# Kernel optimization log

Measured on AMD Instinct MI355X. Metric: run time of the kernel, lower is better.

## Reference

```python
import jax, jax.numpy as jnp
import numpy as np

SIGMA = 0.4


def setup_inputs() -> dict:
    key = jax.random.key(0)
    k1, k2, k3 = jax.random.split(key, 3)
    B, T_out, T_in = 64, 2048, 512
    att_ws = jax.random.uniform(k1, (B, T_out, T_in), dtype=jnp.float32)
    ilens = jax.random.randint(k2, (B,), 1, T_in + 1, dtype=jnp.int64)
    olens = jax.random.randint(k3, (B,), 1, T_out + 1, dtype=jnp.int64)
    return {"att_ws": att_ws, "ilens": ilens, "olens": olens}


def reference(att_ws, ilens, olens):
    B, T_out, T_in = att_ws.shape
    dt = att_ws.dtype
    # grid_x indexes output frames (rows), grid_y indexes input tokens (cols)
    gx = jnp.arange(T_out, dtype=dt)[None, :, None]   # [1, T_out, 1]
    gy = jnp.arange(T_in, dtype=dt)[None, None, :]    # [1, 1, T_in]
    il = ilens.astype(dt)[:, None, None]              # [B, 1, 1]
    ol = olens.astype(dt)[:, None, None]
    # guided diagonal mask: 1 - exp(-(y/ilen - x/olen)^2 / (2 sigma^2))
    guided = 1.0 - jnp.exp(-((gy / il - gx / ol) ** 2) / (2.0 * SIGMA ** 2))
    # non-padded region per sample (out_mask & in_mask)
    valid = (gx < ol) & (gy < il)                     # [B, T_out, T_in] bool
    l1_err = jnp.where(valid, guided * att_ws, jnp.zeros((), dt))
    denom = olens.astype(dt)
    l1_mae = l1_err.sum(axis=(1, 2)) / denom
    l2_mse = (l1_err ** 2).sum(axis=(1, 2)) / denom
    return (l1_mae, l2_mse)
```

## Files before the change

kernel.cpp:

```cpp
#include <hip/hip_runtime.h>
#include <hip/hip_bf16.h>


#define GA_B     64
#define GA_TOUT  2048
#define GA_TIN   512
#define ROWS_PER_WAVE   8
#define WAVES_PER_BLOCK 4
#define ROWS_PER_BLOCK  (ROWS_PER_WAVE * WAVES_PER_BLOCK)
#define BLOCK_THREADS   256
#define GRID_X          (GA_TOUT / ROWS_PER_BLOCK)
#define KS 2.1233046f

__global__ __launch_bounds__(BLOCK_THREADS)
void ga_partial_kernel(const float* __restrict__ att,
                       const int* __restrict__ ilens,
                       const int* __restrict__ olens,
                       float* __restrict__ part) {
    const int b    = blockIdx.y;
    const int lane = threadIdx.x & 63;
    const int wave = threadIdx.x >> 6;
    const int waveRow = blockIdx.x * ROWS_PER_BLOCK + wave * ROWS_PER_WAVE;

    const int ol = olens[b];
    const int il = ilens[b];
    const int nv = (il + 3) >> 2;

    float l1 = 0.0f, l2 = 0.0f;

    if (waveRow < ol) {
        const float inv_il_s = KS / (float)il;
        const float inv_ol_s = KS / (float)ol;
        const bool  hi       = (nv > 64);
        const float4* __restrict__ base =
            (const float4*)(att + (size_t)b * GA_TOUT * GA_TIN);

        float ys0[4], ys1[4], m0[4], m1[4];
        #pragma unroll
        for (int j = 0; j < 4; ++j) {
            const int y0 = (lane << 2) + j;
            const int y1 = y0 + 256;
            ys0[j] = (float)y0 * inv_il_s;
            ys1[j] = (float)y1 * inv_il_s;
            m0[j]  = (y0 < il) ? 1.0f : 0.0f;
            m1[j]  = (y1 < il) ? 1.0f : 0.0f;
        }

        float4 A0[ROWS_PER_WAVE], A1[ROWS_PER_WAVE];
        #pragma unroll
        for (int r = 0; r < ROWS_PER_WAVE; ++r) {
            A0[r] = make_float4(0.f, 0.f, 0.f, 0.f);
            A1[r] = make_float4(0.f, 0.f, 0.f, 0.f);
            const int x = waveRow + r;
            if (x < ol) {
                const float4* __restrict__ rowp = base + (size_t)x * (GA_TIN / 4);
                if (lane < nv)              A0[r] = rowp[lane];
                if (hi && (lane + 64 < nv)) A1[r] = rowp[lane + 64];
            }
        }

        #pragma unroll
        for (int r = 0; r < ROWS_PER_WAVE; ++r) {
            const int   x   = waveRow + r;
            const float gxs = (float)x * inv_ol_s;
            {
                const float4 a = A0[r];
                #pragma unroll
                for (int j = 0; j < 4; ++j) {
                    const float av = (j == 0) ? a.x : (j == 1) ? a.y
                                   : (j == 2) ? a.z : a.w;
                    const float w  = ys0[j] - gxs;
                    const float E  = exp2f(-w * w);
                    const float q  = av - av * E;
                    const float e  = q * m0[j];
                    l1 += e;
                    l2 += e * e;
                }
            }
            if (hi) {
                const float4 a = A1[r];
                #pragma unroll
                for (int j = 0; j < 4; ++j) {
                    const float av = (j == 0) ? a.x : (j == 1) ? a.y
                                   : (j == 2) ? a.z : a.w;
                    const float w  = ys1[j] - gxs;
                    const float E  = exp2f(-w * w);
                    const float q  = av - av * E;
                    const float e  = q * m1[j];
                    l1 += e;
                    l2 += e * e;
                }
            }
        }
    }

    #pragma unroll
    for (int o = 32; o > 0; o >>= 1) {
        l1 += __shfl_down(l1, o, 64);
        l2 += __shfl_down(l2, o, 64);
    }
    __shared__ float s1[WAVES_PER_BLOCK];
    __shared__ float s2[WAVES_PER_BLOCK];
    if (lane == 0) { s1[wave] = l1; s2[wave] = l2; }
    __syncthreads();
    if (threadIdx.x == 0) {
        l1 = s1[0] + s1[1] + s1[2] + s1[3];
        l2 = s2[0] + s2[1] + s2[2] + s2[3];
        const int pidx = (b * GRID_X + blockIdx.x) * 2;
        part[pidx + 0] = l1;
        part[pidx + 1] = l2;
    }
}

__global__ __launch_bounds__(64)
void ga_final_kernel(const float* __restrict__ part,
                     const int* __restrict__ olens,
                     float* __restrict__ out) {
    const int b = blockIdx.x;
    const int t = threadIdx.x;
    const float2 p = ((const float2*)part)[b * GRID_X + t];
    float l1 = p.x, l2 = p.y;
    #pragma unroll
    for (int o = 32; o > 0; o >>= 1) {
        l1 += __shfl_down(l1, o, 64);
        l2 += __shfl_down(l2, o, 64);
    }
    if (t == 0) {
        const float d = (float)olens[b];
        out[b]        = l1 / d;
        out[GA_B + b] = l2 / d;
    }
}

extern "C" void kernel_launch(void* const* d_in, const int* in_sizes, int n_in,
                              void* d_out, int out_size, void* d_ws, size_t ws_size,
                              hipStream_t stream) {
    const float* att   = (const float*)d_in[0];
    const int*   ilens = (const int*)d_in[1];
    const int*   olens = (const int*)d_in[2];
    float*       out   = (float*)d_out;
    float*       part  = (float*)d_ws;

    dim3 grid1(GRID_X, GA_B);
    ga_partial_kernel<<<grid1, BLOCK_THREADS, 0, stream>>>(att, ilens, olens, part);
    ga_final_kernel<<<GA_B, 64, 0, stream>>>(part, olens, out);
}
```

Measured before the change: 25.94 us.

## Remap lanes to 4 rows x 16 column chunks with 64-column window granularity

Each wave now covers 4 rows at a time, with 16 lanes per row each loading a float4, and walks up to 8 windows of 64 columns. Loads and compute stop at ceil(il/64) windows, so short sequences waste fewer lanes than the old 256-column granularity. The column mask is applied only in the last partial window, which removes per-element mask multiplies in full windows. The cost is more branching per window and twice as many load instructions per row.

Result: faster. 22.25 us (-14.2%).

```diff
diff --git a/kernel.cpp b/kernel.cpp
--- a/kernel.cpp
+++ b/kernel.cpp
@@ -16,7 +16,7 @@
 void ga_partial_kernel(const float* __restrict__ att,
                        const int* __restrict__ ilens,
                        const int* __restrict__ olens,
-                       float* __restrict__ part) {
+                       float2* __restrict__ part) {
     const int b    = blockIdx.y;
     const int lane = threadIdx.x & 63;
     const int wave = threadIdx.x >> 6;
@@ -24,71 +24,87 @@
 
     const int ol = olens[b];
     const int il = ilens[b];
-    const int nv = (il + 3) >> 2;
 
     float l1 = 0.0f, l2 = 0.0f;
 
     if (waveRow < ol) {
+        const int q = lane >> 4;
+        const int l = lane & 15;
+        const int full_w = il >> 6;
+        const int nw     = (il + 63) >> 6;
+
         const float inv_il_s = KS / (float)il;
         const float inv_ol_s = KS / (float)ol;
-        const bool  hi       = (nv > 64);
-        const float4* __restrict__ base =
-            (const float4*)(att + (size_t)b * GA_TOUT * GA_TIN);
+        const float* __restrict__ bbase = att + (size_t)b * GA_TOUT * GA_TIN;
 
-        float ys0[4], ys1[4], m0[4], m1[4];
+        int   row[2];
+        float gx[2];
+        #pragma unroll
+        for (int g = 0; g < 2; ++g) {
+            row[g] = waveRow + g * 4 + q;
+            gx[g]  = (float)row[g] * inv_ol_s;
+        }
+
+        float ysb[4];
+        #pragma unroll
+        for (int j = 0; j < 4; ++j)
+            ysb[j] = (float)((l << 2) + j) * inv_il_s;
+
+        float mb[4];
         #pragma unroll
         for (int j = 0; j < 4; ++j) {
-            const int y0 = (lane << 2) + j;
-            const int y1 = y0 + 256;
-            ys0[j] = (float)y0 * inv_il_s;
-            ys1[j] = (float)y1 * inv_il_s;
-            m0[j]  = (y0 < il) ? 1.0f : 0.0f;
-            m1[j]  = (y1 < il) ? 1.0f : 0.0f;
+            const int col = (full_w << 6) + (l << 2) + j;
+            mb[j] = (col < il) ? 1.0f : 0.0f;
         }
 
-        float4 A0[ROWS_PER_WAVE], A1[ROWS_PER_WAVE];
+        float4 A[2][8];
         #pragma unroll
-        for (int r = 0; r < ROWS_PER_WAVE; ++r) {
-            A0[r] = make_float4(0.f, 0.f, 0.f, 0.f);
-            A1[r] = make_float4(0.f, 0.f, 0.f, 0.f);
-            const int x = waveRow + r;
-            if (x < ol) {
-                const float4* __restrict__ rowp = base + (size_t)x * (GA_TIN / 4);
-                if (lane < nv)              A0[r] = rowp[lane];
-                if (hi && (lane + 64 < nv)) A1[r] = rowp[lane + 64];
+        for (int w = 0; w < 8; ++w) {
+            #pragma unroll
+            for (int g = 0; g < 2; ++g) {
+                A[g][w] = make_float4(0.f, 0.f, 0.f, 0.f);
+                if (w < nw && row[g] < ol) {
+                    A[g][w] = ((const float4*)(bbase + (size_t)row[g] * GA_TIN))
+                              [(w << 4) + l];
+                }
             }
         }
 
         #pragma unroll
-        for (int r = 0; r < ROWS_PER_WAVE; ++r) {
-            const int   x   = waveRow + r;
-            const float gxs = (float)x * inv_ol_s;
-            {
-                const float4 a = A0[r];
+        for (int w = 0; w < 8; ++w) {
+            if (w < full_w) {
+                const float off = (float)(w << 6) * inv_il_s;
                 #pragma unroll
-                for (int j = 0; j < 4; ++j) {
-                    const float av = (j == 0) ? a.x : (j == 1) ? a.y
-                                   : (j == 2) ? a.z : a.w;
-                    const float w  = ys0[j] - gxs;
-                    const float E  = exp2f(-w * w);
-                    const float q  = av - av * E;
-                    const float e  = q * m0[j];
-                    l1 += e;
-                    l2 += e * e;
+                for (int g = 0; g < 2; ++g) {
+                    const float  c = off - gx[g];
+                    const float4 a = A[g][w];
+                    #pragma unroll
+                    for (int j = 0; j < 4; ++j) {
+                        const float av = (j == 0) ? a.x : (j == 1) ? a.y
+                                       : (j == 2) ? a.z : a.w;
+                        const float wv = ysb[j] + c;
+                        const float E  = exp2f(-wv * wv);
+                        const float e  = av - av * E;
+                        l1 += e;
+                        l2 += e * e;
+                    }
                 }
-            }
-            if (hi) {
-                const float4 a = A1[r];
+            } else if (w < nw) {
+                const float off = (float)(w << 6) * inv_il_s;
                 #pragma unroll
-                for (int j = 0; j < 4; ++j) {
-                    const float av = (j == 0) ? a.x : (j == 1) ? a.y
-                                   : (j == 2) ? a.z : a.w;
-                    const float w  = ys1[j] - gxs;
-                    const float E  = exp2f(-w * w);
-                    const float q  = av - av * E;
-                    const float e  = q * m1[j];
-                    l1 += e;
-                    l2 += e * e;
+                for (int g = 0; g < 2; ++g) {
+                    const float  c = off - gx[g];
+                    const float4 a = A[g][w];
+                    #pragma unroll
+                    for (int j = 0; j < 4; ++j) {
+                        const float av = (j == 0) ? a.x : (j == 1) ? a.y
+                                       : (j == 2) ? a.z : a.w;
+                        const float wv = ysb[j] + c;
+                        const float E  = exp2f(-wv * wv);
+                        const float e  = (av - av * E) * mb[j];
+                        l1 += e;
+                        l2 += e * e;
+                    }
                 }
             }
         }
@@ -104,21 +120,19 @@
     if (lane == 0) { s1[wave] = l1; s2[wave] = l2; }
     __syncthreads();
     if (threadIdx.x == 0) {
-        l1 = s1[0] + s1[1] + s1[2] + s1[3];
-        l2 = s2[0] + s2[1] + s2[2] + s2[3];
-        const int pidx = (b * GRID_X + blockIdx.x) * 2;
-        part[pidx + 0] = l1;
-        part[pidx + 1] = l2;
+        const float b1 = s1[0] + s1[1] + s1[2] + s1[3];
+        const float b2 = s2[0] + s2[1] + s2[2] + s2[3];
+        part[b * GRID_X + blockIdx.x] = make_float2(b1, b2);
     }
 }
 
 __global__ __launch_bounds__(64)
-void ga_final_kernel(const float* __restrict__ part,
+void ga_final_kernel(const float2* __restrict__ part,
                      const int* __restrict__ olens,
                      float* __restrict__ out) {
     const int b = blockIdx.x;
     const int t = threadIdx.x;
-    const float2 p = ((const float2*)part)[b * GRID_X + t];
+    const float2 p = part[b * GRID_X + t];
     float l1 = p.x, l2 = p.y;
     #pragma unroll
     for (int o = 32; o > 0; o >>= 1) {
@@ -139,7 +153,7 @@
     const int*   ilens = (const int*)d_in[1];
     const int*   olens = (const int*)d_in[2];
     float*       out   = (float*)d_out;
-    float*       part  = (float*)d_ws;
+    float2*      part  = (float2*)d_ws;
 
     dim3 grid1(GRID_X, GA_B);
     ga_partial_kernel<<<grid1, BLOCK_THREADS, 0, stream>>>(att, ilens, olens, part);
```
